# Optimization experiments

Measured on AMD Instinct MI355X. Metric: run time of the kernel, lower is better.

The kernel has to match this reference:

```python
import jax, jax.numpy as jnp
import numpy as np

SEQ_LEN = 128   # sourceL == seq_len
BATCH   = 256
E_DIM   = 512
H_DIM   = 512
C_EXPL  = 10.0  # tanh_exploration


def setup_inputs() -> dict:
    key = jax.random.key(0)
    ks = jax.random.split(key, 24)
    rn = lambda k, shape, s=0.05: (jax.random.normal(k, shape, jnp.float32) * s)
    inp = {
        'decoder_input':  rn(ks[0], (BATCH, E_DIM), 1.0),
        'embedded_inputs': rn(ks[1], (SEQ_LEN, BATCH, E_DIM), 1.0),
        'h0': rn(ks[2], (BATCH, H_DIM), 1.0),
        'c0': rn(ks[3], (BATCH, H_DIM), 1.0),
        'context': rn(ks[4], (SEQ_LEN, BATCH, H_DIM), 1.0),
        # LSTM cell weights (nn.Linear: y = x @ W.T + b)
        'Wi': rn(ks[5], (4 * H_DIM, E_DIM)), 'bi': rn(ks[6], (4 * H_DIM,)),
        'Wh': rn(ks[7], (4 * H_DIM, H_DIM)), 'bh': rn(ks[8], (4 * H_DIM,)),
        # glimpse attention (use_tanh=False)
        'g_Wq': rn(ks[9], (H_DIM, H_DIM)),  'g_bq': rn(ks[10], (H_DIM,)),
        'g_Wref': rn(ks[11], (H_DIM, H_DIM)), 'g_bref': rn(ks[12], (H_DIM,)),
        'g_v': rn(ks[13], (H_DIM,), 1.0 / np.sqrt(H_DIM)),
        # pointer attention (use_tanh=True, C=10)
        'p_Wq': rn(ks[14], (H_DIM, H_DIM)),  'p_bq': rn(ks[15], (H_DIM,)),
        'p_Wref': rn(ks[16], (H_DIM, H_DIM)), 'p_bref': rn(ks[17], (H_DIM,)),
        'p_v': rn(ks[18], (H_DIM,), 1.0 / np.sqrt(H_DIM)),
    }
    return inp


def reference(decoder_input, embedded_inputs, h0, c0, context,
              Wi, bi, Wh, bh,
              g_Wq, g_bq, g_Wref, g_bref, g_v,
              p_Wq, p_bq, p_Wref, p_bref, p_v):
    L, B, H = context.shape

    # Conv1d(k=1) on ref is loop-invariant: precompute e = W_ref @ context, [B,H,L]
    e_g = jnp.einsum('oh,lbh->bol', g_Wref, context) + g_bref[None, :, None]
    e_p = jnp.einsum('oh,lbh->bol', p_Wref, context) + p_bref[None, :, None]
    barange = jnp.arange(B)

    def step(carry, key):
        hx, cx, dec_in, mask, prev = carry
        # fused LSTM cell
        gates = dec_in @ Wi.T + bi + hx @ Wh.T + bh
        i_, f_, g_, o_ = jnp.split(gates, 4, axis=1)
        cy = jax.nn.sigmoid(f_) * cx + jax.nn.sigmoid(i_) * jnp.tanh(g_)
        hy = jax.nn.sigmoid(o_) * jnp.tanh(cy)
        # mark previously selected index as visited
        mask = mask.at[barange, prev].set(True)
        # glimpse (n_glimpses=1, use_tanh=False)
        q = hy @ g_Wq.T + g_bq                                   # [B,H]
        u = jnp.einsum('h,bhl->bl', g_v, jnp.tanh(q[:, :, None] + e_g))
        u = jnp.where(mask, -jnp.inf, u)
        g_l = jnp.einsum('bhl,bl->bh', e_g, jax.nn.softmax(u, axis=1))
        # pointer (use_tanh=True): logits = C * tanh(u), then mask
        q = g_l @ p_Wq.T + p_bq
        u = jnp.einsum('h,bhl->bl', p_v, jnp.tanh(q[:, :, None] + e_p))
        u = jnp.where(mask, -jnp.inf, C_EXPL * jnp.tanh(u))
        probs = jax.nn.softmax(u, axis=1)                        # [B,L]
        # stochastic decode: multinomial sample, gather next embedding
        idxs = jax.random.categorical(key, u, axis=1)            # [B]
        dec_next = embedded_inputs[idxs, barange, :]             # [B,E]
        return (hy, cy, dec_next, mask, idxs), (probs, idxs)

    mask0 = jnp.zeros((B, L), dtype=bool).at[:, 0].set(True)
    prev0 = jnp.zeros((B,), dtype=jnp.int32)
    keys = jax.random.split(jax.random.key(1), L - 1)
    (hy, cy, _, _, _), (probs_seq, idxs_seq) = jax.lax.scan(
        step, (h0, c0, decoder_input, mask0, prev0), keys)

    prob_0 = jnp.zeros((B, L), jnp.float32).at[:, 0].set(1.0)
    outputs = jnp.concatenate([prob_0[None], probs_seq], axis=0)          # [L,B,L]
    selections = jnp.concatenate([prev0[None], idxs_seq], axis=0)         # [L,B]
    return outputs, selections, hy, cy
```

## Files before the change

### kernel.cpp

```cpp
#include <hip/hip_runtime.h>
#include <stdint.h>

#ifndef THREEFRY_PARTITIONABLE
#define THREEFRY_PARTITIONABLE 1
#endif

#define LSEQ 128
#define BSZ  256
#define HD   512
#define G4   2048

#define SEL_OFF  ((size_t)LSEQ * BSZ * LSEQ)
#define HY_OFF   (SEL_OFF + (size_t)LSEQ * BSZ)
#define CY_OFF   (HY_OFF + (size_t)BSZ * HD)

__device__ __forceinline__ uint32_t rotl_(uint32_t v, int r) { return (v << r) | (v >> (32 - r)); }

__device__ __forceinline__ void tf2x32(uint32_t k0, uint32_t k1,
                                       uint32_t x0, uint32_t x1,
                                       uint32_t &o0, uint32_t &o1)
{
  uint32_t k2 = k0 ^ k1 ^ 0x1BD11BDAu;
  x0 += k0; x1 += k1;
#define TFR(r) { x0 += x1; x1 = rotl_(x1,(r)); x1 ^= x0; }
  TFR(13) TFR(15) TFR(26) TFR(6)
  x0 += k1; x1 += k2 + 1u;
  TFR(17) TFR(29) TFR(16) TFR(24)
  x0 += k2; x1 += k0 + 2u;
  TFR(13) TFR(15) TFR(26) TFR(6)
  x0 += k0; x1 += k1 + 3u;
  TFR(17) TFR(29) TFR(16) TFR(24)
  x0 += k1; x1 += k2 + 4u;
  TFR(13) TFR(15) TFR(26) TFR(6)
  x0 += k2; x1 += k0 + 5u;
#undef TFR
  o0 = x0; o1 = x1;
}

__device__ __forceinline__ void step_key(int t, uint32_t &kA, uint32_t &kB)
{
#if THREEFRY_PARTITIONABLE
  uint32_t o0, o1;
  tf2x32(0u, 1u, 0u, (uint32_t)t, o0, o1);
  kA = o0; kB = o1;
#else
  uint32_t o0, o1;
  uint32_t j = 2u * (uint32_t)t;
  if (j < 127u) { tf2x32(0u, 1u, j, 127u + j, o0, o1); kA = o0; }
  else          { tf2x32(0u, 1u, j - 127u, j, o0, o1); kA = o1; }
  j = 2u * (uint32_t)t + 1u;
  if (j < 127u) { tf2x32(0u, 1u, j, 127u + j, o0, o1); kB = o0; }
  else          { tf2x32(0u, 1u, j - 127u, j, o0, o1); kB = o1; }
#endif
}

__device__ __forceinline__ uint32_t draw_bits(uint32_t kA, uint32_t kB, uint32_t n)
{
  uint32_t y0, y1;
#if THREEFRY_PARTITIONABLE
  tf2x32(kA, kB, 0u, n, y0, y1);
  return y0 ^ y1;
#else
  uint32_t i0 = (n < 16384u) ? n : n - 16384u;
  tf2x32(kA, kB, i0, i0 + 16384u, y0, y1);
  return (n < 16384u) ? y0 : y1;
#endif
}

__device__ __forceinline__ double tanh_c(double x)
{
  float xf = (float)x;
  float ax = fabsf(xf);
  float z  = fminf(ax * 2.8853900817779268f, 50.0f);
  float e  = exp2f(z);
  float r  = 2.0f / (e + 1.0f);
  float t  = copysignf(1.0f - r, xf);
  float dx = (float)(x - (double)xf);
  return (double)t + (double)((1.0f - t * t) * dx);
}

template<int RM, int CHUNK>
__global__ __launch_bounds__(256)
void gemm32(const float* __restrict__ A0, const float* __restrict__ A1, int lda,
            const float* __restrict__ B0, const float* __restrict__ B1, int ldb,
            const float* __restrict__ bias,
            double* __restrict__ Cd0, double* __restrict__ Cd1,
            float* __restrict__ Cf0, float* __restrict__ Cf1,
            int N, int K, int out_mode)
{
  constexpr int BM = RM * 16;
  constexpr int BN = 64;
  constexpr int BK = 32;
  __shared__ float As[BK][BM];
  __shared__ float Bs[BK][BN];
  const int tid = threadIdx.x;
  const int tx = tid & 15, ty = tid >> 4;
  const int z = blockIdx.z;
  const float* A = z ? A1 : A0;
  const float* B = z ? B1 : B0;
  const int m0 = blockIdx.x * BM;
  const int n0 = blockIdx.y * BN;

  const int b_r = tid >> 2, b_kq = (tid & 3) * 8;
  const int a_r  = (RM == 4) ? (tid >> 2) : (tid >> 3);
  const int a_kq = (RM == 4) ? ((tid & 3) * 8) : ((tid & 7) * 4);

  double acc[RM][4];
  float  c32[RM][4];
#pragma unroll
  for (int i = 0; i < RM; ++i)
#pragma unroll
    for (int j = 0; j < 4; ++j) { acc[i][j] = 0.0; c32[i][j] = 0.0f; }

  const float* bp0 = B + (size_t)(n0 + b_r) * ldb + b_kq;
  float4 w0 = *(const float4*)bp0;
  float4 w1 = *(const float4*)(bp0 + 4);
  const float* ap0 = A + (size_t)(m0 + a_r) * lda + a_kq;
  float4 u0 = *(const float4*)ap0;
  float4 u1 = (RM == 4) ? *(const float4*)(ap0 + 4) : u0;

  for (int k0 = 0; k0 < K; k0 += BK) {
    __syncthreads();
    Bs[b_kq + 0][b_r] = w0.x; Bs[b_kq + 1][b_r] = w0.y;
    Bs[b_kq + 2][b_r] = w0.z; Bs[b_kq + 3][b_r] = w0.w;
    Bs[b_kq + 4][b_r] = w1.x; Bs[b_kq + 5][b_r] = w1.y;
    Bs[b_kq + 6][b_r] = w1.z; Bs[b_kq + 7][b_r] = w1.w;
    As[a_kq + 0][a_r] = u0.x; As[a_kq + 1][a_r] = u0.y;
    As[a_kq + 2][a_r] = u0.z; As[a_kq + 3][a_r] = u0.w;
    if (RM == 4) {
      As[a_kq + 4][a_r] = u1.x; As[a_kq + 5][a_r] = u1.y;
      As[a_kq + 6][a_r] = u1.z; As[a_kq + 7][a_r] = u1.w;
    }
    __syncthreads();

    float4 nw0 = w0, nw1 = w1, nu0 = u0, nu1 = u1;
    if (k0 + BK < K) {
      const float* bp = B + (size_t)(n0 + b_r) * ldb + (k0 + BK) + b_kq;
      nw0 = *(const float4*)bp;
      nw1 = *(const float4*)(bp + 4);
      const float* ap = A + (size_t)(m0 + a_r) * lda + (k0 + BK) + a_kq;
      nu0 = *(const float4*)ap;
      if (RM == 4) nu1 = *(const float4*)(ap + 4);
    }

#pragma unroll
    for (int kk = 0; kk < BK; ++kk) {
      float a[RM];
      if (RM == 4) {
        float4 av = *(const float4*)&As[kk][4 * ty];
        a[0] = av.x; a[1] = av.y; a[2] = av.z; a[3] = av.w;
      } else {
        float2 av = *(const float2*)&As[kk][2 * ty];
        a[0] = av.x; a[1] = av.y;
      }
      float4 bv = *(const float4*)&Bs[kk][4 * tx];
#pragma unroll
      for (int i = 0; i < RM; ++i) {
        c32[i][0] = fmaf(a[i], bv.x, c32[i][0]);
        c32[i][1] = fmaf(a[i], bv.y, c32[i][1]);
        c32[i][2] = fmaf(a[i], bv.z, c32[i][2]);
        c32[i][3] = fmaf(a[i], bv.w, c32[i][3]);
      }
      if ((kk & (CHUNK - 1)) == (CHUNK - 1)) {
#pragma unroll
        for (int i = 0; i < RM; ++i)
#pragma unroll
          for (int j = 0; j < 4; ++j) { acc[i][j] += (double)c32[i][j]; c32[i][j] = 0.0f; }
      }
    }
    w0 = nw0; w1 = nw1; u0 = nu0; u1 = nu1;
  }

#pragma unroll
  for (int i = 0; i < RM; ++i) {
    int m = m0 + RM * ty + i;
#pragma unroll
    for (int j = 0; j < 4; ++j) {
      int n = n0 + 4 * tx + j;
      double v = acc[i][j] + (bias ? (double)bias[n] : 0.0);
      if (out_mode == 0) {
        double* Cd = z ? Cd1 : Cd0;
        Cd[(size_t)m * N + n] = v;
      } else if (out_mode == 1) {
        Cf0[(((size_t)(m & 255)) * LSEQ + (m >> 8)) * HD + n] = (float)v;
      } else if (out_mode == 2) {
        Cf0[(size_t)m * N + n] = (float)v;
      } else if (out_mode == 3) {
        Cf0[(((size_t)(m & 255)) * HD + n) * LSEQ + (m >> 8)] = (float)v;
      } else {
        float* Cf = z ? Cf1 : Cf0;
        Cf[(size_t)m * N + n] = (float)v;
      }
    }
  }
}

__global__ __launch_bounds__(256)
void transpose512(const float* __restrict__ W, float* __restrict__ WT)
{
  __shared__ float tile[32][33];
  int bx = blockIdx.x * 32, by = blockIdx.y * 32;
  int x = threadIdx.x & 31, y = threadIdx.x >> 5;
#pragma unroll
  for (int j = 0; j < 32; j += 8)
    tile[y + j][x] = W[(size_t)(by + y + j) * HD + bx + x];
  __syncthreads();
#pragma unroll
  for (int j = 0; j < 32; j += 8)
    WT[(size_t)(bx + y + j) * HD + by + x] = tile[x][y + j];
}

__global__ __launch_bounds__(512)
void vecmat512(const float* __restrict__ W, const float* __restrict__ x,
               float* __restrict__ y)
{
  int h = threadIdx.x;
  double a = 0.0;
  for (int k0 = 0; k0 < HD; k0 += 8) {
    float c = 0.0f;
#pragma unroll
    for (int j = 0; j < 8; ++j)
      c = fmaf(W[(size_t)h * HD + k0 + j], x[k0 + j], c);
    a += (double)c;
  }
  y[h] = (float)a;
}

#define SCOMP(A0_, A1_, A2_, A3_, V4, IT)                         \
  {                                                               \
    const int h_ = (IT) * 16 + hh;                                \
    double xq_ = qs[h_];                                          \
    double vv_ = (double)vs[h_];                                  \
    A0_ += vv_ * tanh_c(xq_ + (double)(V4).x);                    \
    A1_ += vv_ * tanh_c(xq_ + (double)(V4).y);                    \
    A2_ += vv_ * tanh_c(xq_ + (double)(V4).z);                    \
    A3_ += vv_ * tanh_c(xq_ + (double)(V4).w);                    \
  }

__global__ __launch_bounds__(512)
void step_fused(const float* __restrict__ g0, const float* __restrict__ g1,
                const float* __restrict__ bi, const float* __restrict__ bh,
                const double* __restrict__ c_in, double* __restrict__ c_out,
                float* __restrict__ h_out,
                const float* __restrict__ WqT, const float* __restrict__ g_bq,
                const float* __restrict__ e_g, const float* __restrict__ F,
                const float* __restrict__ e_p,
                const float* __restrict__ g_v, const float* __restrict__ p_v,
                const float* __restrict__ p_bq,
                unsigned char* __restrict__ mask,
                const float* __restrict__ emb, float* __restrict__ dec_in,
                float* __restrict__ out, int t)
{
  const int b   = blockIdx.x;
  const int tid = threadIdx.x;
  const int l   = tid & 127;
  const int lg  = tid & 31;
  const int hh  = tid >> 5;
  __shared__ float  hs[HD];
  __shared__ double qs[HD];
  __shared__ float  vs[HD];
  __shared__ double part[16][LSEQ];
  __shared__ double sarr[LSEQ];
  __shared__ double red[4];
  __shared__ double wv[2];
  __shared__ int    wi[2];
  __shared__ int    selidx;

  const float* egbase = e_g + (size_t)b * (HD * LSEQ) + hh * LSEQ + lg * 4;
  const float* epbase = e_p + (size_t)b * (HD * LSEQ) + hh * LSEQ + lg * 4;

  float4 B0[8], B1[8];
#pragma unroll
  for (int j = 0; j < 8; ++j)
    B0[j] = *(const float4*)(egbase + (size_t)j * (16 * LSEQ));

  {
    const int u = tid;
    const size_t base = (size_t)b * G4;
    double gi = (double)g0[base + u]        + (double)g1[base + u]        + (double)bi[u]        + (double)bh[u];
    double gf = (double)g0[base + u + 512]  + (double)g1[base + u + 512]  + (double)bi[u + 512]  + (double)bh[u + 512];
    double gg = (double)g0[base + u + 1024] + (double)g1[base + u + 1024] + (double)bi[u + 1024] + (double)bh[u + 1024];
    double go = (double)g0[base + u + 1536] + (double)g1[base + u + 1536] + (double)bi[u + 1536] + (double)bh[u + 1536];
    double si = 1.0 / (1.0 + exp(-gi));
    double sf = 1.0 / (1.0 + exp(-gf));
    double so = 1.0 / (1.0 + exp(-go));
    double cy = sf * c_in[(size_t)b * HD + u] + si * tanh(gg);
    double hy = so * tanh(cy);
    c_out[(size_t)b * HD + u] = cy;
    float hyf = (float)hy;
    h_out[(size_t)b * HD + u] = hyf;
    hs[u] = hyf;
  }
  __syncthreads();

  {
    const int h = tid;
    const float* wcol = WqT + h;
    float wA[32], wB[32];
    double a = 0.0;
#pragma unroll
    for (int j = 0; j < 32; ++j) wA[j] = wcol[(size_t)j * HD];
#pragma unroll
    for (int pair = 0; pair < 8; ++pair) {
      const int kA = pair * 64;
#pragma unroll
      for (int j = 0; j < 32; ++j) wB[j] = wcol[(size_t)(kA + 32 + j) * HD];
#pragma unroll
      for (int c = 0; c < 4; ++c) {
        float c32 = 0.0f;
#pragma unroll
        for (int j = 0; j < 8; ++j)
          c32 = fmaf(hs[kA + c * 8 + j], wA[c * 8 + j], c32);
        a += (double)c32;
      }
      if (pair < 7) {
#pragma unroll
        for (int j = 0; j < 32; ++j) wA[j] = wcol[(size_t)(kA + 64 + j) * HD];
      }
#pragma unroll
      for (int c = 0; c < 4; ++c) {
        float c32 = 0.0f;
#pragma unroll
        for (int j = 0; j < 8; ++j)
          c32 = fmaf(hs[kA + 32 + c * 8 + j], wB[c * 8 + j], c32);
        a += (double)c32;
      }
    }
    qs[tid] = a + (double)g_bq[tid];
    vs[tid] = g_v[tid];
  }
  __syncthreads();

  {
    double a0 = 0, a1 = 0, a2 = 0, a3 = 0;
#pragma unroll
    for (int j = 0; j < 8; ++j)
      B1[j] = *(const float4*)(egbase + (size_t)(8 + j) * (16 * LSEQ));
#pragma unroll
    for (int j = 0; j < 8; ++j) SCOMP(a0, a1, a2, a3, B0[j], j);
#pragma unroll
    for (int j = 0; j < 8; ++j)
      B0[j] = *(const float4*)(egbase + (size_t)(16 + j) * (16 * LSEQ));
#pragma unroll
    for (int j = 0; j < 8; ++j) SCOMP(a0, a1, a2, a3, B1[j], 8 + j);
#pragma unroll
    for (int j = 0; j < 8; ++j)
      B1[j] = *(const float4*)(egbase + (size_t)(24 + j) * (16 * LSEQ));
#pragma unroll
    for (int j = 0; j < 8; ++j) SCOMP(a0, a1, a2, a3, B0[j], 16 + j);
#pragma unroll
    for (int j = 0; j < 8; ++j) SCOMP(a0, a1, a2, a3, B1[j], 24 + j);
    part[hh][lg * 4 + 0] = a0;
    part[hh][lg * 4 + 1] = a1;
    part[hh][lg * 4 + 2] = a2;
    part[hh][lg * 4 + 3] = a3;
  }
  __syncthreads();

  bool   msk = false;
  double u = 0.0, pe = 0.0;
  if (tid < 128) {
    msk = mask[(size_t)b * LSEQ + l] != 0;
    u = 0.0;
#pragma unroll
    for (int o = 0; o < 16; ++o) u += part[o][l];
    if (msk) u = -__builtin_inf();
    double mx = u;
    for (int off = 32; off; off >>= 1) mx = fmax(mx, __shfl_xor(mx, off));
    if ((tid & 63) == 0) red[tid >> 6] = mx;
  }
  __syncthreads();
  if (tid < 128) {
    double mx = fmax(red[0], red[1]);
    pe = msk ? 0.0 : exp(u - mx);
    double sm = pe;
    for (int off = 32; off; off >>= 1) sm += __shfl_xor(sm, off);
    if ((tid & 63) == 0) red[2 + (tid >> 6)] = sm;
  }
  __syncthreads();
  if (tid < 128) sarr[l] = pe / (red[2] + red[3]);
  __syncthreads();

  {
    const float* Fb = F + (size_t)b * LSEQ * HD + tid;
#pragma unroll
    for (int j = 0; j < 8; ++j)
      B0[j] = *(const float4*)(epbase + (size_t)j * (16 * LSEQ));

    float fA[32], fB[32];
    double a = 0.0;
#pragma unroll
    for (int j = 0; j < 32; ++j) fA[j] = Fb[(size_t)j * HD];
#pragma unroll
    for (int pair = 0; pair < 2; ++pair) {
      const int llA = pair * 64;
#pragma unroll
      for (int j = 0; j < 32; ++j) fB[j] = Fb[(size_t)(llA + 32 + j) * HD];
#pragma unroll
      for (int j = 0; j < 32; ++j) a += (double)fA[j] * sarr[llA + j];
      if (pair < 1) {
#pragma unroll
        for (int j = 0; j < 32; ++j) fA[j] = Fb[(size_t)(llA + 64 + j) * HD];
      }
#pragma unroll
      for (int j = 0; j < 32; ++j) a += (double)fB[j] * sarr[llA + 32 + j];
    }
    qs[tid] = a + (double)p_bq[tid];
    vs[tid] = p_v[tid];
  }
  __syncthreads();

  {
    double a0 = 0, a1 = 0, a2 = 0, a3 = 0;
#pragma unroll
    for (int j = 0; j < 8; ++j)
      B1[j] = *(const float4*)(epbase + (size_t)(8 + j) * (16 * LSEQ));
#pragma unroll
    for (int j = 0; j < 8; ++j) SCOMP(a0, a1, a2, a3, B0[j], j);
#pragma unroll
    for (int j = 0; j < 8; ++j)
      B0[j] = *(const float4*)(epbase + (size_t)(16 + j) * (16 * LSEQ));
#pragma unroll
    for (int j = 0; j < 8; ++j) SCOMP(a0, a1, a2, a3, B1[j], 8 + j);
#pragma unroll
    for (int j = 0; j < 8; ++j)
      B1[j] = *(const float4*)(epbase + (size_t)(24 + j) * (16 * LSEQ));
#pragma unroll
    for (int j = 0; j < 8; ++j) SCOMP(a0, a1, a2, a3, B0[j], 16 + j);
#pragma unroll
    for (int j = 0; j < 8; ++j) SCOMP(a0, a1, a2, a3, B1[j], 24 + j);
    part[hh][lg * 4 + 0] = a0;
    part[hh][lg * 4 + 1] = a1;
    part[hh][lg * 4 + 2] = a2;
    part[hh][lg * 4 + 3] = a3;
  }
  __syncthreads();

  double logit = 0.0, cand = 0.0;
  int idx = l;
  if (tid < 128) {
    double acc2 = 0.0;
#pragma unroll
    for (int o = 0; o < 16; ++o) acc2 += part[o][l];
    logit = msk ? -__builtin_inf() : 10.0 * tanh(acc2);
    double mx = logit;
    for (int off = 32; off; off >>= 1) mx = fmax(mx, __shfl_xor(mx, off));
    if ((tid & 63) == 0) red[tid >> 6] = mx;
  }
  __syncthreads();
  if (tid < 128) {
    double mx = fmax(red[0], red[1]);
    double pe2 = msk ? 0.0 : exp(logit - mx);
    double sm = pe2;
    for (int off = 32; off; off >>= 1) sm += __shfl_xor(sm, off);
    if ((tid & 63) == 0) red[2 + (tid >> 6)] = sm;
    __threadfence_block();
  }
  __syncthreads();
  if (tid < 128) {
    double mx = fmax(red[0], red[1]);
    double pe2 = msk ? 0.0 : exp(logit - mx);
    out[(size_t)(t + 1) * BSZ * LSEQ + (size_t)b * LSEQ + l] = (float)(pe2 / (red[2] + red[3]));

    uint32_t kA, kB;
    step_key(t, kA, kB);
    uint32_t bits = draw_bits(kA, kB, (uint32_t)(b * LSEQ + l));
    float f = __uint_as_float((bits >> 9) | 0x3f800000u) - 1.0f;
    const float TINY = 1.17549435e-38f;
    float uu = fmaxf(f * (1.0f - TINY) + TINY, TINY);
    float gmb = -logf(-logf(uu));
    cand = msk ? -__builtin_inf() : (logit + (double)gmb);

    for (int off = 32; off; off >>= 1) {
      double c2 = __shfl_xor(cand, off);
      int    i2 = __shfl_xor(idx, off);
      if (c2 > cand || (c2 == cand && i2 < idx)) { cand = c2; idx = i2; }
    }
    if ((tid & 63) == 0) { wv[tid >> 6] = cand; wi[tid >> 6] = idx; }
  }
  __syncthreads();
  if (tid == 0) {
    double c2 = wv[1]; int i2 = wi[1];
    if (c2 > cand || (c2 == cand && i2 < idx)) { cand = c2; idx = i2; }
    selidx = idx;
    out[SEL_OFF + (size_t)(t + 1) * BSZ + b] = (float)idx;
    mask[(size_t)b * LSEQ + idx] = 1;
  }
  __syncthreads();
  {
    int sidx = selidx;
    dec_in[(size_t)b * HD + tid] = emb[((size_t)sidx * BSZ + b) * HD + tid];
  }
}

__global__ __launch_bounds__(256)
void init_kernel(const float* __restrict__ dec0, const float* __restrict__ h0,
                 const float* __restrict__ c0, float* __restrict__ dec_in,
                 float* __restrict__ hf, double* __restrict__ c,
                 unsigned char* __restrict__ mask, float* __restrict__ out)
{
  int i = blockIdx.x * blockDim.x + threadIdx.x;
  if (i < BSZ * HD) { hf[i] = h0[i]; c[i] = (double)c0[i]; dec_in[i] = dec0[i]; }
  if (i < BSZ * LSEQ) {
    mask[i] = ((i & (LSEQ - 1)) == 0) ? 1 : 0;
    out[i] = ((i & (LSEQ - 1)) == 0) ? 1.0f : 0.0f;
  }
  if (i < BSZ) out[SEL_OFF + i] = 0.0f;
}

__global__ __launch_bounds__(256)
void finalize(const float* __restrict__ hf, const double* __restrict__ c,
              float* __restrict__ out)
{
  int i = blockIdx.x * blockDim.x + threadIdx.x;
  if (i < BSZ * HD) {
    out[HY_OFF + i] = hf[i];
    out[CY_OFF + i] = (float)c[i];
  }
}

extern "C" void kernel_launch(void* const* d_in, const int* in_sizes, int n_in,
                              void* d_out, int out_size, void* d_ws, size_t ws_size,
                              hipStream_t stream)
{
  (void)in_sizes; (void)n_in; (void)out_size; (void)ws_size;
  const float* dec0  = (const float*)d_in[0];
  const float* emb   = (const float*)d_in[1];
  const float* h0    = (const float*)d_in[2];
  const float* c0    = (const float*)d_in[3];
  const float* ctx   = (const float*)d_in[4];
  const float* Wi    = (const float*)d_in[5];
  const float* bi    = (const float*)d_in[6];
  const float* Wh    = (const float*)d_in[7];
  const float* bh    = (const float*)d_in[8];
  const float* gWq   = (const float*)d_in[9];
  const float* gbq   = (const float*)d_in[10];
  const float* gWref = (const float*)d_in[11];
  const float* gbref = (const float*)d_in[12];
  const float* gv    = (const float*)d_in[13];
  const float* pWq   = (const float*)d_in[14];
  const float* pbq   = (const float*)d_in[15];
  const float* pWref = (const float*)d_in[16];
  const float* pbref = (const float*)d_in[17];
  const float* pv    = (const float*)d_in[18];
  float* out = (float*)d_out;

  char* ws = (char*)d_ws;
  size_t off = 0;
  auto take = [&](size_t bytes) -> char* {
    char* p = ws + off;
    off += (bytes + 255) & ~(size_t)255;
    return p;
  };
  float*  e_g   = (float*) take((size_t)BSZ * LSEQ * HD * 4);
  float*  e_p   = (float*) take((size_t)BSZ * LSEQ * HD * 4);
  float*  Fq2   = (float*) take((size_t)BSZ * LSEQ * HD * 4);
  float*  g0f   = (float*) take((size_t)BSZ * G4 * 4);
  float*  g1f   = (float*) take((size_t)BSZ * G4 * 4);
  double* cb0   = (double*)take((size_t)BSZ * HD * 8);
  double* cb1   = (double*)take((size_t)BSZ * HD * 8);
  float*  hf0   = (float*) take((size_t)BSZ * HD * 4);
  float*  hf1   = (float*) take((size_t)BSZ * HD * 4);
  float*  WqT   = (float*) take((size_t)HD * HD * 4);
  float*  WrefT = (float*) take((size_t)HD * HD * 4);
  float*  W2    = (float*) take((size_t)HD * HD * 4);
  float*  b2    = (float*) take((size_t)HD * 4);
  float*  decb  = (float*) take((size_t)BSZ * HD * 4);
  unsigned char* mask = (unsigned char*)take((size_t)BSZ * LSEQ);

  init_kernel<<<512, 256, 0, stream>>>(dec0, h0, c0, decb, hf0, cb0, mask, out);
  transpose512<<<dim3(16, 16), 256, 0, stream>>>(gWq, WqT);
  transpose512<<<dim3(16, 16), 256, 0, stream>>>(gWref, WrefT);
  gemm32<4, 8><<<dim3(HD / 64, HD / 64, 1), 256, 0, stream>>>(
      pWq, nullptr, HD, WrefT, nullptr, HD, nullptr,
      nullptr, nullptr, W2, nullptr, HD, HD, 2);
  vecmat512<<<1, 512, 0, stream>>>(pWq, gbref, b2);

  gemm32<4, 8><<<dim3(BSZ * LSEQ / 64, HD / 64, 1), 256, 0, stream>>>(
      ctx, nullptr, HD, gWref, nullptr, HD, gbref,
      nullptr, nullptr, e_g, nullptr, HD, HD, 3);
  gemm32<4, 8><<<dim3(BSZ * LSEQ / 64, HD / 64, 1), 256, 0, stream>>>(
      ctx, nullptr, HD, pWref, nullptr, HD, pbref,
      nullptr, nullptr, e_p, nullptr, HD, HD, 3);
  gemm32<4, 8><<<dim3(BSZ * LSEQ / 64, HD / 64, 1), 256, 0, stream>>>(
      ctx, nullptr, HD, W2, nullptr, HD, b2,
      nullptr, nullptr, Fq2, nullptr, HD, HD, 1);

  double* cb[2] = { cb0, cb1 };
  float*  hf[2] = { hf0, hf1 };
  for (int t = 0; t < LSEQ - 1; ++t) {
    int rs = t & 1, wsl = rs ^ 1;
    gemm32<4, 8><<<dim3(BSZ / 64, G4 / 64, 2), 256, 0, stream>>>(
        decb, hf[rs], HD, Wi, Wh, HD, nullptr,
        nullptr, nullptr, g0f, g1f, G4, HD, 4);
    step_fused<<<BSZ, 512, 0, stream>>>(g0f, g1f, bi, bh,
                                        cb[rs], cb[wsl], hf[wsl],
                                        WqT, gbq, e_g, Fq2, e_p, gv, pv, pbq,
                                        mask, emb, decb, out, t);
  }
  finalize<<<BSZ * HD / 256, 256, 0, stream>>>(hf[1], cb[1], out);
}
```

Before: 13.64 ms.

## Replace precomputed folded pointer-query tensor with per-step glimpse then Wq matvec

Drops the precomputed F = context·(p_Wq·g_Wref)ᵀ tensor (BSZ×LSEQ×HD) and its setup GEMMs. Each step now computes the glimpse g_l = e_g·softmax directly from e_g rows, then multiplies by a transposed p_Wq inside step_fused. This removes a large setup GEMM and a 64MB buffer, but adds a 512×512 matvec per block per step that reads the whole weight matrix, mostly from cache. Separately, tanh_c now uses hardware exp2 and a reciprocal refined by one Newton step instead of a full-precision divide.

```diff
diff --git a/kernel.cpp b/kernel.cpp
--- a/kernel.cpp
+++ b/kernel.cpp
@@ -72,9 +72,11 @@
   float xf = (float)x;
   float ax = fabsf(xf);
   float z  = fminf(ax * 2.8853900817779268f, 50.0f);
-  float e  = exp2f(z);
-  float r  = 2.0f / (e + 1.0f);
-  float t  = copysignf(1.0f - r, xf);
+  float e  = __builtin_amdgcn_exp2f(z);
+  float d  = e + 1.0f;
+  float r0 = __builtin_amdgcn_rcpf(d);
+  float r  = fmaf(fmaf(-d, r0, 1.0f), r0, r0);
+  float t  = copysignf(fmaf(-2.0f, r, 1.0f), xf);
   float dx = (float)(x - (double)xf);
   return (double)t + (double)((1.0f - t * t) * dx);
 }
@@ -210,22 +212,6 @@
     WT[(size_t)(bx + y + j) * HD + by + x] = tile[x][y + j];
 }
 
-__global__ __launch_bounds__(512)
-void vecmat512(const float* __restrict__ W, const float* __restrict__ x,
-               float* __restrict__ y)
-{
-  int h = threadIdx.x;
-  double a = 0.0;
-  for (int k0 = 0; k0 < HD; k0 += 8) {
-    float c = 0.0f;
-#pragma unroll
-    for (int j = 0; j < 8; ++j)
-      c = fmaf(W[(size_t)h * HD + k0 + j], x[k0 + j], c);
-    a += (double)c;
-  }
-  y[h] = (float)a;
-}
-
 #define SCOMP(A0_, A1_, A2_, A3_, V4, IT)                         \
   {                                                               \
     const int h_ = (IT) * 16 + hh;                                \
@@ -243,10 +229,10 @@
                 const double* __restrict__ c_in, double* __restrict__ c_out,
                 float* __restrict__ h_out,
                 const float* __restrict__ WqT, const float* __restrict__ g_bq,
-                const float* __restrict__ e_g, const float* __restrict__ F,
+                const float* __restrict__ e_g,
+                const float* __restrict__ pWqT, const float* __restrict__ p_bq,
                 const float* __restrict__ e_p,
                 const float* __restrict__ g_v, const float* __restrict__ p_v,
-                const float* __restrict__ p_bq,
                 unsigned char* __restrict__ mask,
                 const float* __restrict__ emb, float* __restrict__ dec_in,
                 float* __restrict__ out, int t)
@@ -260,6 +246,7 @@
   __shared__ double qs[HD];
   __shared__ float  vs[HD];
   __shared__ double part[16][LSEQ];
+  __shared__ double gls[HD];
   __shared__ double sarr[LSEQ];
   __shared__ double red[4];
   __shared__ double wv[2];
@@ -382,28 +369,65 @@
   __syncthreads();
 
   {
-    const float* Fb = F + (size_t)b * LSEQ * HD + tid;
 #pragma unroll
     for (int j = 0; j < 8; ++j)
       B0[j] = *(const float4*)(epbase + (size_t)j * (16 * LSEQ));
 
-    float fA[32], fB[32];
+    const float4* row = (const float4*)(e_g + ((size_t)b * HD + tid) * LSEQ);
+    float4 rA[4], rB[4];
     double a = 0.0;
 #pragma unroll
-    for (int j = 0; j < 32; ++j) fA[j] = Fb[(size_t)j * HD];
-#pragma unroll
-    for (int pair = 0; pair < 2; ++pair) {
-      const int llA = pair * 64;
-#pragma unroll
-      for (int j = 0; j < 32; ++j) fB[j] = Fb[(size_t)(llA + 32 + j) * HD];
-#pragma unroll
-      for (int j = 0; j < 32; ++j) a += (double)fA[j] * sarr[llA + j];
-      if (pair < 1) {
-#pragma unroll
-        for (int j = 0; j < 32; ++j) fA[j] = Fb[(size_t)(llA + 64 + j) * HD];
-      }
-#pragma unroll
-      for (int j = 0; j < 32; ++j) a += (double)fB[j] * sarr[llA + 32 + j];
+    for (int j = 0; j < 4; ++j) rA[j] = row[j];
+#pragma unroll
+    for (int r = 0; r < 4; ++r) {
+#pragma unroll
+      for (int j = 0; j < 4; ++j) rB[j] = row[r * 8 + 4 + j];
+#pragma unroll
+      for (int j = 0; j < 4; ++j) {
+        int l4 = (r * 8 + j) * 4;
+        float4 v = rA[j];
+        a += (double)v.x * sarr[l4 + 0];
+        a += (double)v.y * sarr[l4 + 1];
+        a += (double)v.z * sarr[l4 + 2];
+        a += (double)v.w * sarr[l4 + 3];
+      }
+      if (r < 3) {
+#pragma unroll
+        for (int j = 0; j < 4; ++j) rA[j] = row[r * 8 + 8 + j];
+      }
+#pragma unroll
+      for (int j = 0; j < 4; ++j) {
+        int l4 = (r * 8 + 4 + j) * 4;
+        float4 v = rB[j];
+        a += (double)v.x * sarr[l4 + 0];
+        a += (double)v.y * sarr[l4 + 1];
+        a += (double)v.z * sarr[l4 + 2];
+        a += (double)v.w * sarr[l4 + 3];
+      }
+    }
+    gls[tid] = a;
+  }
+  __syncthreads();
+
+  {
+    const float* wcol = pWqT + tid;
+    float wA[32], wB[32];
+    double a = 0.0;
+#pragma unroll
+    for (int j = 0; j < 32; ++j) wA[j] = wcol[(size_t)j * HD];
+#pragma unroll
+    for (int pair = 0; pair < 8; ++pair) {
+      const int hA = pair * 64;
+#pragma unroll
+      for (int j = 0; j < 32; ++j) wB[j] = wcol[(size_t)(hA + 32 + j) * HD];
+#pragma unroll
+      for (int j = 0; j < 32; ++j) a += gls[hA + j] * (double)wA[j];
+      if (pair < 7) {
+#pragma unroll
+        for (int j = 0; j < 32; ++j) wA[j] = wcol[(size_t)(hA + 64 + j) * HD];
+      }
+#pragma unroll
+      for (int j = 0; j < 32; ++j) a += gls[hA + 32 + j] * (double)wB[j];
     }
     qs[tid] = a + (double)p_bq[tid];
     vs[tid] = p_v[tid];
@@ -554,7 +578,6 @@
   };
   float*  e_g   = (float*) take((size_t)BSZ * LSEQ * HD * 4);
   float*  e_p   = (float*) take((size_t)BSZ * LSEQ * HD * 4);
-  float*  Fq2   = (float*) take((size_t)BSZ * LSEQ * HD * 4);
   float*  g0f   = (float*) take((size_t)BSZ * G4 * 4);
   float*  g1f   = (float*) take((size_t)BSZ * G4 * 4);
   double* cb0   = (double*)take((size_t)BSZ * HD * 8);
@@ -562,19 +585,13 @@
   float*  hf0   = (float*) take((size_t)BSZ * HD * 4);
   float*  hf1   = (float*) take((size_t)BSZ * HD * 4);
   float*  WqT   = (float*) take((size_t)HD * HD * 4);
-  float*  WrefT = (float*) take((size_t)HD * HD * 4);
-  float*  W2    = (float*) take((size_t)HD * HD * 4);
-  float*  b2    = (float*) take((size_t)HD * 4);
+  float*  pWqT  = (float*) take((size_t)HD * HD * 4);
   float*  decb  = (float*) take((size_t)BSZ * HD * 4);
   unsigned char* mask = (unsigned char*)take((size_t)BSZ * LSEQ);
 
   init_kernel<<<512, 256, 0, stream>>>(dec0, h0, c0, decb, hf0, cb0, mask, out);
   transpose512<<<dim3(16, 16), 256, 0, stream>>>(gWq, WqT);
-  transpose512<<<dim3(16, 16), 256, 0, stream>>>(gWref, WrefT);
-  gemm32<4, 8><<<dim3(HD / 64, HD / 64, 1), 256, 0, stream>>>(
-      pWq, nullptr, HD, WrefT, nullptr, HD, nullptr,
-      nullptr, nullptr, W2, nullptr, HD, HD, 2);
-  vecmat512<<<1, 512, 0, stream>>>(pWq, gbref, b2);
+  transpose512<<<dim3(16, 16), 256, 0, stream>>>(pWq, pWqT);
 
   gemm32<4, 8><<<dim3(BSZ * LSEQ / 64, HD / 64, 1), 256, 0, stream>>>(
       ctx, nullptr, HD, gWref, nullptr, HD, gbref,
@@ -582,9 +599,6 @@
   gemm32<4, 8><<<dim3(BSZ * LSEQ / 64, HD / 64, 1), 256, 0, stream>>>(
       ctx, nullptr, HD, pWref, nullptr, HD, pbref,
       nullptr, nullptr, e_p, nullptr, HD, HD, 3);
-  gemm32<4, 8><<<dim3(BSZ * LSEQ / 64, HD / 64, 1), 256, 0, stream>>>(
-      ctx, nullptr, HD, W2, nullptr, HD, b2,
-      nullptr, nullptr, Fq2, nullptr, HD, HD, 1);
 
   double* cb[2] = { cb0, cb1 };
   float*  hf[2] = { hf0, hf1 };
@@ -595,7 +609,7 @@
         nullptr, nullptr, g0f, g1f, G4, HD, 4);
     step_fused<<<BSZ, 512, 0, stream>>>(g0f, g1f, bi, bh,
                                         cb[rs], cb[wsl], hf[wsl],
-                                        WqT, gbq, e_g, Fq2, e_p, gv, pv, pbq,
+                                        WqT, gbq, e_g, pWqT, pbq, e_p, gv, pv,
                                         mask, emb, decb, out, t);
   }
   finalize<<<BSZ * HD / 256, 256, 0, stream>>>(hf[1], cb[1], out);
```

Measured after the change: 13.70 ms. About the same (+0.4%).
